# Optimization experiments

Measured on AMD Instinct MI355X. Metric: run time of the kernel, lower is better.

Reference implementation:

```python
import jax, jax.numpy as jnp
import numpy as np

B, N_PER, C, KG, KTOP, KNN = 8, 2048, 256, 16, 512, 32
N = B * N_PER
E = N * KG
EPS = 1e-5


def setup_inputs() -> dict:
    key = jax.random.key(0)
    ks = jax.random.split(key, 32)
    s = 0.05
    x = jax.random.normal(ks[0], (N, C), jnp.float32)
    x_origin = jax.random.normal(ks[1], (N, C), jnp.float32)
    xyz = jax.random.uniform(ks[2], (N, 3), jnp.float32)
    # graph: every node is a dst with KG incoming edges from random nodes of the SAME sample
    edge_dst = jnp.repeat(jnp.arange(N, dtype=jnp.int32), KG)
    src_local = jax.random.randint(ks[3], (E,), 0, N_PER, dtype=jnp.int32)
    edge_src = src_local + (edge_dst // N_PER) * N_PER
    # EdgeConv params (theta on x_j - x_i, phi on x_i)
    theta_w = jax.random.normal(ks[4], (C, C), jnp.float32) * s
    theta_b = jax.random.normal(ks[5], (C,), jnp.float32) * s
    phi_w = jax.random.normal(ks[6], (C, C), jnp.float32) * s
    phi_b = jax.random.normal(ks[7], (C,), jnp.float32) * s
    # region_score_mlp: Conv1d(C,64,1)-ReLU-BN(64)-Conv1d(64,32,1)-ReLU-BN(32)-Conv1d(32,1,1)
    w1 = jax.random.normal(ks[8], (64, C), jnp.float32) * s
    b1 = jax.random.normal(ks[9], (64,), jnp.float32) * s
    g1 = 1.0 + 0.1 * jax.random.normal(ks[10], (64,), jnp.float32)
    be1 = 0.1 * jax.random.normal(ks[11], (64,), jnp.float32)
    m1 = 0.1 * jax.random.normal(ks[12], (64,), jnp.float32)
    v1 = jax.random.uniform(ks[13], (64,), jnp.float32, 0.5, 1.5)
    w2 = jax.random.normal(ks[14], (32, 64), jnp.float32) * s
    b2 = jax.random.normal(ks[15], (32,), jnp.float32) * s
    g2 = 1.0 + 0.1 * jax.random.normal(ks[16], (32,), jnp.float32)
    be2 = 0.1 * jax.random.normal(ks[17], (32,), jnp.float32)
    m2 = 0.1 * jax.random.normal(ks[18], (32,), jnp.float32)
    v2 = jax.random.uniform(ks[19], (32,), jnp.float32, 0.5, 1.5)
    w3 = jax.random.normal(ks[20], (1, 32), jnp.float32) * s
    b3 = jax.random.normal(ks[21], (1,), jnp.float32) * s
    return dict(x=x, x_origin=x_origin, xyz=xyz, edge_src=edge_src, edge_dst=edge_dst,
                theta_w=theta_w, theta_b=theta_b, phi_w=phi_w, phi_b=phi_b,
                w1=w1, b1=b1, g1=g1, be1=be1, m1=m1, v1=v1,
                w2=w2, b2=b2, g2=g2, be2=be2, m2=m2, v2=v2, w3=w3, b3=b3)


def _bn(t, g, b, m, v):
    return (t - m) * jax.lax.rsqrt(v + EPS) * g + b


def _forward(x, x_origin, xyz, edge_src, edge_dst,
             theta_w, theta_b, phi_w, phi_b,
             w1, b1, g1, be1, m1, v1, w2, b2, g2, be2, m2, v2, w3, b3):
    # EdgeConv: h_i = max_{j->i}( theta(x_j - x_i) + phi(x_i) ), then residual add
    msg = ((x[edge_src] - x[edge_dst]) @ theta_w.T + theta_b
           + x[edge_dst] @ phi_w.T + phi_b)                      # [E, C]
    h = jax.ops.segment_max(msg, edge_dst, num_segments=N)       # [N, C]
    x1 = h + x                                                   # residual
    # per-node MLP (Conv1d kernel-size 1 == linear), BN in eval mode
    t = _bn(jax.nn.relu(x1 @ w1.T + b1), g1, be1, m1, v1)
    t = _bn(jax.nn.relu(t @ w2.T + b2), g2, be2, m2, v2)
    score = t @ w3.T + b3                                        # [N, 1]
    score_b = score.reshape(B, N_PER)                            # vps_score
    # per-batch top-k (cls=False path: select by raw score, descending)
    topk_vals, topk_idx = jax.lax.top_k(score_b, KTOP)           # [B, KTOP]
    perm = (topk_idx + jnp.arange(B, dtype=topk_idx.dtype)[:, None] * N_PER).reshape(-1)
    x_new = x1[perm].reshape(B, KTOP, C)
    x_copy = x_origin[perm].reshape(B, KTOP, -1)
    xyz_sel = xyz[perm].reshape(B, KTOP, 3)
    # rebuild 32-NN graph per sample on selected points (batched, no per-b python calls)
    d2 = jnp.sum((xyz_sel[:, :, None, :] - xyz_sel[:, None, :, :]) ** 2, axis=-1)  # [B,K,K]
    _, knn_idx = jax.lax.top_k(-d2, KNN)                         # [B, KTOP, 32]
    return knn_idx, x_new, x_copy, score_b, topk_vals


def reference(x, x_origin, xyz, edge_src, edge_dst,
              theta_w, theta_b, phi_w, phi_b,
              w1, b1, g1, be1, m1, v1, w2, b2, g2, be2, m2, v2, w3, b3):
    return _forward(x, x_origin, xyz, edge_src, edge_dst,
                    theta_w, theta_b, phi_w, phi_b,
                    w1, b1, g1, be1, m1, v1, w2, b2, g2, be2, m2, v2, w3, b3)
```

## Files before the change

### kernel.cpp

```cpp
#include <hip/hip_runtime.h>
#include <math.h>

constexpr int B     = 8;
constexpr int N_PER = 2048;
constexpr int C     = 256;
constexpr int KG    = 16;
constexpr int KTOP  = 512;
constexpr int KNN   = 32;
constexpr int N     = B * N_PER;
constexpr float EPS = 1e-5f;

typedef __attribute__((ext_vector_type(8))) short  short8;
typedef __attribute__((ext_vector_type(4))) float  f32x4;

__device__ inline void split3(float f, unsigned short& h, unsigned short& m,
                              unsigned short& l)
{
    const unsigned u  = __float_as_uint(f);
    const unsigned r1 = (u + 0x7FFFu + ((u >> 16) & 1u)) & 0xFFFF0000u;
    h = (unsigned short)(r1 >> 16);
    const float f2 = f - __uint_as_float(r1);
    const unsigned u2 = __float_as_uint(f2);
    const unsigned r2 = (u2 + 0x7FFFu + ((u2 >> 16) & 1u)) & 0xFFFF0000u;
    m = (unsigned short)(r2 >> 16);
    const float f3 = f2 - __uint_as_float(r2);
    const unsigned u3 = __float_as_uint(f3);
    l = (unsigned short)((u3 + 0x7FFFu + ((u3 >> 16) & 1u)) >> 16);
}

__device__ inline void cvt_store24(unsigned short* dh, unsigned short* dm,
                                   unsigned short* dl, float4 a, float4 b)
{
    short8 h, m, l;
    unsigned short hh, mm, ll;
    float v[8] = {a.x, a.y, a.z, a.w, b.x, b.y, b.z, b.w};
#pragma unroll
    for (int j = 0; j < 8; ++j) {
        split3(v[j], hh, mm, ll);
        h[j] = (short)hh;
        m[j] = (short)mm;
        l[j] = (short)ll;
    }
    *(short8*)dh = h;
    *(short8*)dm = m;
    *(short8*)dl = l;
}

__device__ inline void split8v(const float* __restrict__ s,
                               unsigned short* __restrict__ dh,
                               unsigned short* __restrict__ dm,
                               unsigned short* __restrict__ dl)
{
    float4 a = *(const float4*)s;
    float4 b = *(const float4*)(s + 4);
    float v[8] = {a.x, a.y, a.z, a.w, b.x, b.y, b.z, b.w};
    short8 h8, m8, l8;
    unsigned short hh, mm, ll;
#pragma unroll
    for (int j = 0; j < 8; ++j) {
        split3(v[j], hh, mm, ll);
        h8[j] = (short)hh;
        m8[j] = (short)mm;
        l8[j] = (short)ll;
    }
    *(short8*)dh = h8;
    *(short8*)dm = m8;
    *(short8*)dl = l8;
}

constexpr int GW = C * C / 8;

__global__ __launch_bounds__(256) void k0w_split(
    const float* __restrict__ thw, const float* __restrict__ phw,
    unsigned short* __restrict__ th, unsigned short* __restrict__ tm,
    unsigned short* __restrict__ tl,
    unsigned short* __restrict__ ph, unsigned short* __restrict__ pm,
    unsigned short* __restrict__ pl)
{
    const int g = blockIdx.x * 256 + threadIdx.x;
    if (g < GW) {
        const int o = g * 8;
        split8v(thw + o, th + o, tm + o, tl + o);
    } else if (g < 2 * GW) {
        const int o = (g - GW) * 8;
        split8v(phw + o, ph + o, pm + o, pl + o);
    }
}

__global__ __launch_bounds__(256) void k1_wp(
    const float* __restrict__ x,
    const unsigned short* __restrict__ th, const unsigned short* __restrict__ tm,
    const unsigned short* __restrict__ tl,
    const unsigned short* __restrict__ ph, const unsigned short* __restrict__ pm,
    const unsigned short* __restrict__ pl,
    const float* __restrict__ thb, const float* __restrict__ phb,
    float* __restrict__ T, float* __restrict__ R)
{
    constexpr int BM = 128, BN = 64, ST = 40;
    __shared__ unsigned short sA[3][BM * ST];
    __shared__ unsigned short sT[3][BN * ST];
    __shared__ unsigned short sP[3][BN * ST];

    const int tid  = threadIdx.x;
    const int row0 = blockIdx.x * BM;
    const int n0   = blockIdx.y * BN;
    const int lane = tid & 63;
    const int wv   = tid >> 6;
    const int wr   = (wv >> 1) * 64;
    const int wc   = (wv & 1) * 32;
    const int fr   = lane & 15;
    const int fk   = (lane >> 4) * 8;
    const int ar0  = tid >> 2;
    const int ac   = (tid & 3) * 8;

    f32x4 acTh[4][2], acTl[4][2], acQh[4][2], acQl[4][2];
    const f32x4 zz = {0.f, 0.f, 0.f, 0.f};
#pragma unroll
    for (int m = 0; m < 4; ++m)
#pragma unroll
        for (int n = 0; n < 2; ++n) {
            acTh[m][n] = zz; acTl[m][n] = zz;
            acQh[m][n] = zz; acQl[m][n] = zz;
        }

    const float* xA0 = x + (size_t)(row0 + ar0)      * C + ac;
    const float* xA1 = x + (size_t)(row0 + 64 + ar0) * C + ac;
    const size_t offW = (size_t)(n0 + ar0) * C + ac;

    float4 a0a = *(const float4*)(xA0 + 0), a0b = *(const float4*)(xA0 + 4);
    float4 a1a = *(const float4*)(xA1 + 0), a1b = *(const float4*)(xA1 + 4);
    short8 rTh = *(const short8*)(th + offW);
    short8 rTm = *(const short8*)(tm + offW);
    short8 rTl = *(const short8*)(tl + offW);
    short8 rPh = *(const short8*)(ph + offW);
    short8 rPm = *(const short8*)(pm + offW);
    short8 rPl = *(const short8*)(pl + offW);

    const int sOffA0 = ar0 * ST + ac;
    const int sOffA1 = (64 + ar0) * ST + ac;
    const int aBase  = (wr + fr) * ST + fk;
    const int bBase  = (wc + fr) * ST + fk;

    for (int step = 0; step < 8; ++step) {
        __syncthreads();
        cvt_store24(sA[0] + sOffA0, sA[1] + sOffA0, sA[2] + sOffA0, a0a, a0b);
        cvt_store24(sA[0] + sOffA1, sA[1] + sOffA1, sA[2] + sOffA1, a1a, a1b);
        *(short8*)(sT[0] + sOffA0) = rTh;
        *(short8*)(sT[1] + sOffA0) = rTm;
        *(short8*)(sT[2] + sOffA0) = rTl;
        *(short8*)(sP[0] + sOffA0) = rPh;
        *(short8*)(sP[1] + sOffA0) = rPm;
        *(short8*)(sP[2] + sOffA0) = rPl;
        __syncthreads();

        if (step < 7) {
            const int kn = (step + 1) * 32;
            a0a = *(const float4*)(xA0 + kn); a0b = *(const float4*)(xA0 + kn + 4);
            a1a = *(const float4*)(xA1 + kn); a1b = *(const float4*)(xA1 + kn + 4);
            rTh = *(const short8*)(th + offW + kn);
            rTm = *(const short8*)(tm + offW + kn);
            rTl = *(const short8*)(tl + offW + kn);
            rPh = *(const short8*)(ph + offW + kn);
            rPm = *(const short8*)(pm + offW + kn);
            rPl = *(const short8*)(pl + offW + kn);
        }

        short8 a1f[4], a2f[4], a3f[4];
#pragma unroll
        for (int m = 0; m < 4; ++m) {
            const int r = aBase + m * 16 * ST;
            a1f[m] = *(const short8*)(sA[0] + r);
            a2f[m] = *(const short8*)(sA[1] + r);
            a3f[m] = *(const short8*)(sA[2] + r);
        }
        {
            short8 t0[2], p0[2];
#pragma unroll
            for (int n = 0; n < 2; ++n) {
                const int r = bBase + n * 16 * ST;
                t0[n] = *(const short8*)(sT[0] + r);
                p0[n] = *(const short8*)(sP[0] + r);
            }
#pragma unroll
            for (int m = 0; m < 4; ++m)
#pragma unroll
                for (int n = 0; n < 2; ++n) {
                    acTh[m][n] = __builtin_amdgcn_mfma_f32_16x16x32_bf16(a1f[m], t0[n], acTh[m][n], 0, 0, 0);
                    acQh[m][n] = __builtin_amdgcn_mfma_f32_16x16x32_bf16(a1f[m], p0[n], acQh[m][n], 0, 0, 0);
                    acTl[m][n] = __builtin_amdgcn_mfma_f32_16x16x32_bf16(a2f[m], t0[n], acTl[m][n], 0, 0, 0);
                    acQl[m][n] = __builtin_amdgcn_mfma_f32_16x16x32_bf16(a2f[m], p0[n], acQl[m][n], 0, 0, 0);
                    acTl[m][n] = __builtin_amdgcn_mfma_f32_16x16x32_bf16(a3f[m], t0[n], acTl[m][n], 0, 0, 0);
                    acQl[m][n] = __builtin_amdgcn_mfma_f32_16x16x32_bf16(a3f[m], p0[n], acQl[m][n], 0, 0, 0);
                }
        }
        {
            short8 t1[2], p1[2];
#pragma unroll
            for (int n = 0; n < 2; ++n) {
                const int r = bBase + n * 16 * ST;
                t1[n] = *(const short8*)(sT[1] + r);
                p1[n] = *(const short8*)(sP[1] + r);
            }
#pragma unroll
            for (int m = 0; m < 4; ++m)
#pragma unroll
                for (int n = 0; n < 2; ++n) {
                    acTl[m][n] = __builtin_amdgcn_mfma_f32_16x16x32_bf16(a1f[m], t1[n], acTl[m][n], 0, 0, 0);
                    acQl[m][n] = __builtin_amdgcn_mfma_f32_16x16x32_bf16(a1f[m], p1[n], acQl[m][n], 0, 0, 0);
                    acTl[m][n] = __builtin_amdgcn_mfma_f32_16x16x32_bf16(a2f[m], t1[n], acTl[m][n], 0, 0, 0);
                    acQl[m][n] = __builtin_amdgcn_mfma_f32_16x16x32_bf16(a2f[m], p1[n], acQl[m][n], 0, 0, 0);
                }
        }
        {
            short8 t2[2], p2[2];
#pragma unroll
            for (int n = 0; n < 2; ++n) {
                const int r = bBase + n * 16 * ST;
                t2[n] = *(const short8*)(sT[2] + r);
                p2[n] = *(const short8*)(sP[2] + r);
            }
#pragma unroll
            for (int m = 0; m < 4; ++m)
#pragma unroll
                for (int n = 0; n < 2; ++n) {
                    acTl[m][n] = __builtin_amdgcn_mfma_f32_16x16x32_bf16(a1f[m], t2[n], acTl[m][n], 0, 0, 0);
                    acQl[m][n] = __builtin_amdgcn_mfma_f32_16x16x32_bf16(a1f[m], p2[n], acQl[m][n], 0, 0, 0);
                }
        }
    }

    const int cr = (lane >> 4) * 4;
#pragma unroll
    for (int m = 0; m < 4; ++m) {
#pragma unroll
        for (int n = 0; n < 2; ++n) {
            const int col  = n0 + wc + n * 16 + fr;
            const float bias = thb[col] + phb[col];
#pragma unroll
            for (int j = 0; j < 4; ++j) {
                const int row = row0 + wr + m * 16 + cr + j;
                const size_t off = (size_t)row * C + col;
                const float tval = acTh[m][n][j] + acTl[m][n][j];
                const float qval = acQh[m][n][j] + acQl[m][n][j];
                T[off] = tval;
                R[off] = x[off] + qval + bias - tval;
            }
        }
    }
}

__global__ __launch_bounds__(256) void k1_fb(
    const float* __restrict__ x, const float* __restrict__ thw,
    const float* __restrict__ phw, const float* __restrict__ thb,
    const float* __restrict__ phb, float* __restrict__ T, float* __restrict__ R)
{
    constexpr int BM = 128, BN = 64, ST = 40;
    __shared__ unsigned short sA[3][BM * ST];
    __shared__ unsigned short sT[3][BN * ST];
    __shared__ unsigned short sP[3][BN * ST];

    const int tid  = threadIdx.x;
    const int row0 = blockIdx.x * BM;
    const int n0   = blockIdx.y * BN;
    const int lane = tid & 63;
    const int wv   = tid >> 6;
    const int wr   = (wv >> 1) * 64;
    const int wc   = (wv & 1) * 32;
    const int fr   = lane & 15;
    const int fk   = (lane >> 4) * 8;
    const int ar0 = tid >> 2;
    const int ac  = (tid & 3) * 8;

    f32x4 acTh[4][2], acTl[4][2], acQh[4][2], acQl[4][2];
    const f32x4 zz = {0.f, 0.f, 0.f, 0.f};
#pragma unroll
    for (int m = 0; m < 4; ++m)
#pragma unroll
        for (int n = 0; n < 2; ++n) {
            acTh[m][n] = zz; acTl[m][n] = zz;
            acQh[m][n] = zz; acQl[m][n] = zz;
        }

    const float* xA0 = x   + (size_t)(row0 + ar0)      * C + ac;
    const float* xA1 = x   + (size_t)(row0 + 64 + ar0) * C + ac;
    const float* wT  = thw + (size_t)(n0 + ar0)        * C + ac;
    const float* wP  = phw + (size_t)(n0 + ar0)        * C + ac;

    float4 a0a = *(const float4*)(xA0 + 0), a0b = *(const float4*)(xA0 + 4);
    float4 a1a = *(const float4*)(xA1 + 0), a1b = *(const float4*)(xA1 + 4);
    float4 ta  = *(const float4*)(wT  + 0), tb_ = *(const float4*)(wT  + 4);
    float4 pa  = *(const float4*)(wP  + 0), pb_ = *(const float4*)(wP  + 4);

    const int sOffA0 = ar0 * ST + ac;
    const int sOffA1 = (64 + ar0) * ST + ac;
    const int aBase  = (wr + fr) * ST + fk;
    const int bBase  = (wc + fr) * ST + fk;

    for (int step = 0; step < 8; ++step) {
        __syncthreads();
        cvt_store24(sA[0] + sOffA0, sA[1] + sOffA0, sA[2] + sOffA0, a0a, a0b);
        cvt_store24(sA[0] + sOffA1, sA[1] + sOffA1, sA[2] + sOffA1, a1a, a1b);
        cvt_store24(sT[0] + sOffA0, sT[1] + sOffA0, sT[2] + sOffA0, ta,  tb_);
        cvt_store24(sP[0] + sOffA0, sP[1] + sOffA0, sP[2] + sOffA0, pa,  pb_);
        __syncthreads();

        if (step < 7) {
            const int kn = (step + 1) * 32;
            a0a = *(const float4*)(xA0 + kn); a0b = *(const float4*)(xA0 + kn + 4);
            a1a = *(const float4*)(xA1 + kn); a1b = *(const float4*)(xA1 + kn + 4);
            ta  = *(const float4*)(wT  + kn); tb_ = *(const float4*)(wT  + kn + 4);
            pa  = *(const float4*)(wP  + kn); pb_ = *(const float4*)(wP  + kn + 4);
        }

        short8 a1f[4], a2f[4], a3f[4];
#pragma unroll
        for (int m = 0; m < 4; ++m) {
            const int r = aBase + m * 16 * ST;
            a1f[m] = *(const short8*)(sA[0] + r);
            a2f[m] = *(const short8*)(sA[1] + r);
            a3f[m] = *(const short8*)(sA[2] + r);
        }
        {
            short8 t0[2], p0[2];
#pragma unroll
            for (int n = 0; n < 2; ++n) {
                const int r = bBase + n * 16 * ST;
                t0[n] = *(const short8*)(sT[0] + r);
                p0[n] = *(const short8*)(sP[0] + r);
            }
#pragma unroll
            for (int m = 0; m < 4; ++m)
#pragma unroll
                for (int n = 0; n < 2; ++n) {
                    acTh[m][n] = __builtin_amdgcn_mfma_f32_16x16x32_bf16(a1f[m], t0[n], acTh[m][n], 0, 0, 0);
                    acQh[m][n] = __builtin_amdgcn_mfma_f32_16x16x32_bf16(a1f[m], p0[n], acQh[m][n], 0, 0, 0);
                    acTl[m][n] = __builtin_amdgcn_mfma_f32_16x16x32_bf16(a2f[m], t0[n], acTl[m][n], 0, 0, 0);
                    acQl[m][n] = __builtin_amdgcn_mfma_f32_16x16x32_bf16(a2f[m], p0[n], acQl[m][n], 0, 0, 0);
                    acTl[m][n] = __builtin_amdgcn_mfma_f32_16x16x32_bf16(a3f[m], t0[n], acTl[m][n], 0, 0, 0);
                    acQl[m][n] = __builtin_amdgcn_mfma_f32_16x16x32_bf16(a3f[m], p0[n], acQl[m][n], 0, 0, 0);
                }
        }
        {
            short8 t1[2], p1[2];
#pragma unroll
            for (int n = 0; n < 2; ++n) {
                const int r = bBase + n * 16 * ST;
                t1[n] = *(const short8*)(sT[1] + r);
                p1[n] = *(const short8*)(sP[1] + r);
            }
#pragma unroll
            for (int m = 0; m < 4; ++m)
#pragma unroll
                for (int n = 0; n < 2; ++n) {
                    acTl[m][n] = __builtin_amdgcn_mfma_f32_16x16x32_bf16(a1f[m], t1[n], acTl[m][n], 0, 0, 0);
                    acQl[m][n] = __builtin_amdgcn_mfma_f32_16x16x32_bf16(a1f[m], p1[n], acQl[m][n], 0, 0, 0);
                    acTl[m][n] = __builtin_amdgcn_mfma_f32_16x16x32_bf16(a2f[m], t1[n], acTl[m][n], 0, 0, 0);
                    acQl[m][n] = __builtin_amdgcn_mfma_f32_16x16x32_bf16(a2f[m], p1[n], acQl[m][n], 0, 0, 0);
                }
        }
        {
            short8 t2[2], p2[2];
#pragma unroll
            for (int n = 0; n < 2; ++n) {
                const int r = bBase + n * 16 * ST;
                t2[n] = *(const short8*)(sT[2] + r);
                p2[n] = *(const short8*)(sP[2] + r);
            }
#pragma unroll
            for (int m = 0; m < 4; ++m)
#pragma unroll
                for (int n = 0; n < 2; ++n) {
                    acTl[m][n] = __builtin_amdgcn_mfma_f32_16x16x32_bf16(a1f[m], t2[n], acTl[m][n], 0, 0, 0);
                    acQl[m][n] = __builtin_amdgcn_mfma_f32_16x16x32_bf16(a1f[m], p2[n], acQl[m][n], 0, 0, 0);
                }
        }
    }

    const int cr = (lane >> 4) * 4;
#pragma unroll
    for (int m = 0; m < 4; ++m) {
#pragma unroll
        for (int n = 0; n < 2; ++n) {
            const int col  = n0 + wc + n * 16 + fr;
            const float bias = thb[col] + phb[col];
#pragma unroll
            for (int j = 0; j < 4; ++j) {
                const int row = row0 + wr + m * 16 + cr + j;
                const size_t off = (size_t)row * C + col;
                const float tval = acTh[m][n][j] + acTl[m][n][j];
                const float qval = acQh[m][n][j] + acQl[m][n][j];
                T[off] = tval;
                R[off] = x[off] + qval + bias - tval;
            }
        }
    }
}

__global__ __launch_bounds__(256) void k2ab_fused(
    const int* __restrict__ esrc, const float* __restrict__ T,
    float* __restrict__ x1,
    const float* __restrict__ w1, const float* __restrict__ b1,
    const float* __restrict__ g1, const float* __restrict__ be1,
    const float* __restrict__ m1, const float* __restrict__ v1,
    const float* __restrict__ w2, const float* __restrict__ b2,
    const float* __restrict__ g2, const float* __restrict__ be2,
    const float* __restrict__ m2, const float* __restrict__ v2,
    const float* __restrict__ w3, const float* __restrict__ b3,
    float* __restrict__ score_ws, float* __restrict__ out_score)
{
    constexpr int BK = 16, ST = 68;
    __shared__ float Xs[BK * ST];
    __shared__ float Ws[BK * ST];
    __shared__ float t1s[64 * 65];
    __shared__ float w2s[32 * 65];
    __shared__ float w3s[32];
    __shared__ float zs[64 * 33];
    __shared__ int eidx[64][KG];

    const int tid  = threadIdx.x;
    const int bb   = blockIdx.x & 7;
    const int row0 = bb * N_PER + (blockIdx.x >> 3) * 64;

#pragma unroll
    for (int q = 0; q < 4; ++q) {
        const int i = tid + q * 256;
        eidx[i >> 4][i & 15] = esrc[(row0 + (i >> 4)) * KG + (i & 15)];
    }
    __syncthreads();

    {
        const int w = tid >> 6, c4 = (tid & 63) * 4;
        for (int it = 0; it < 16; ++it) {
            const int nl = w * 16 + it;
            const int g  = row0 + nl;
            float4 acc = make_float4(-INFINITY, -INFINITY, -INFINITY, -INFINITY);
#pragma unroll
            for (int k = 0; k < KG; ++k) {
                const float4 v = *(const float4*)&T[(size_t)eidx[nl][k] * C + c4];
                acc.x = fmaxf(acc.x, v.x);  acc.y = fmaxf(acc.y, v.y);
                acc.z = fmaxf(acc.z, v.z);  acc.w = fmaxf(acc.w, v.w);
            }
            const size_t off = (size_t)g * C + c4;
            float4 r = *(const float4*)&x1[off];
            r.x += acc.x;  r.y += acc.y;  r.z += acc.z;  r.w += acc.w;
            *(float4*)&x1[off] = r;
        }
    }
    __syncthreads();

    const int tx = tid & 15, ty = tid >> 4;
    const int lm = tid >> 2, lq = (tid & 3) << 2;

    float acc[4][4] = {{0.f}};
    for (int k0 = 0; k0 < C; k0 += BK) {
        float4 fx = *(const float4*)(x1 + (size_t)(row0 + lm) * C + k0 + lq);
        float4 fw = *(const float4*)(w1 + (size_t)lm * C + k0 + lq);
        __syncthreads();
        Xs[(lq + 0) * ST + lm] = fx.x;  Xs[(lq + 1) * ST + lm] = fx.y;
        Xs[(lq + 2) * ST + lm] = fx.z;  Xs[(lq + 3) * ST + lm] = fx.w;
        Ws[(lq + 0) * ST + lm] = fw.x;  Ws[(lq + 1) * ST + lm] = fw.y;
        Ws[(lq + 2) * ST + lm] = fw.z;  Ws[(lq + 3) * ST + lm] = fw.w;
        __syncthreads();
#pragma unroll
        for (int k = 0; k < BK; ++k) {
            float4 a4 = *(const float4*)&Xs[k * ST + (ty << 2)];
            float4 w4 = *(const float4*)&Ws[k * ST + (tx << 2)];
            float av[4] = {a4.x, a4.y, a4.z, a4.w};
            float wv[4] = {w4.x, w4.y, w4.z, w4.w};
#pragma unroll
            for (int i2 = 0; i2 < 4; ++i2)
#pragma unroll
                for (int j2 = 0; j2 < 4; ++j2) acc[i2][j2] += av[i2] * wv[j2];
        }
    }
    __syncthreads();
#pragma unroll
    for (int i2 = 0; i2 < 4; ++i2) {
        const int mrow = (ty << 2) + i2;
#pragma unroll
        for (int j2 = 0; j2 < 4; ++j2) {
            const int o = (tx << 2) + j2;
            float y = acc[i2][j2] + b1[o];
            y = fmaxf(y, 0.f);
            y = (y - m1[o]) * (1.0f / sqrtf(v1[o] + EPS)) * g1[o] + be1[o];
            t1s[mrow * 65 + o] = y;
        }
    }
    for (int idx = tid; idx < 2048; idx += 256)
        w2s[(idx >> 6) * 65 + (idx & 63)] = w2[idx];
    if (tid < 32) w3s[tid] = w3[tid];
    __syncthreads();

    const int o = tid & 31;
    const float inv2 = (1.0f / sqrtf(v2[o] + EPS)) * g2[o];
#pragma unroll
    for (int p = 0; p < 8; ++p) {
        const int nl = p * 8 + (tid >> 5);
        float z = 0.f;
#pragma unroll
        for (int j = 0; j < 64; ++j) z += t1s[nl * 65 + j] * w2s[o * 65 + j];
        z += b2[o];
        z = fmaxf(z, 0.f);
        z = (z - m2[o]) * inv2 + be2[o];
        zs[nl * 33 + o] = z;
    }
    __syncthreads();

    if (tid < 64) {
        float sacc = 0.f;
#pragma unroll
        for (int j = 0; j < 32; ++j) sacc += zs[tid * 33 + j] * w3s[j];
        sacc += b3[0];
        const int node = row0 + tid;
        score_ws[node]  = sacc;
        out_score[node] = sacc;
    }
}

__global__ __launch_bounds__(256) void k3_rank(
    const float* __restrict__ score, const float* __restrict__ xyz,
    float* __restrict__ out_topk, int* __restrict__ perm,
    float* __restrict__ xsel)
{
    __shared__ unsigned long long keys[N_PER];
    const int b   = blockIdx.x >> 3;
    const int seg = blockIdx.x & 7;
    const int t   = threadIdx.x;
    for (int i = t; i < N_PER; i += 256) {
        const float v = score[b * N_PER + i];
        unsigned u = __float_as_uint(v);
        const unsigned ua = (u & 0x80000000u) ? ~u : (u | 0x80000000u);
        const unsigned ud = ~ua;
        keys[i] = ((unsigned long long)ud << 32) | (unsigned)i;
    }
    __syncthreads();
    const int i = seg * 256 + t;
    const unsigned long long k = keys[i];
    int r = 0;
#pragma unroll 8
    for (int j = 0; j < N_PER; ++j) r += (keys[j] < k) ? 1 : 0;
    if (r < KTOP) {
        const int g = b * N_PER + i;
        const int o = b * KTOP + r;
        out_topk[o] = score[g];
        perm[o] = g;
        xsel[o * 3 + 0] = xyz[g * 3 + 0];
        xsel[o * 3 + 1] = xyz[g * 3 + 1];
        xsel[o * 3 + 2] = xyz[g * 3 + 2];
    }
}

__device__ inline unsigned long long shfl_xor_u64(unsigned long long v, int m)
{
    unsigned lo = (unsigned)v, hi = (unsigned)(v >> 32);
    lo = __shfl_xor(lo, m, 64);
    hi = __shfl_xor(hi, m, 64);
    return ((unsigned long long)hi << 32) | lo;
}

__global__ __launch_bounds__(256) void k5_rank(
    const int* __restrict__ perm, const float* __restrict__ xsel,
    const float* __restrict__ x1, const float* __restrict__ xorig,
    float* __restrict__ out_xnew, float* __restrict__ out_xcopy,
    float* __restrict__ out_knn)
{
    constexpr int G = 4;
    __shared__ float px[KTOP], py[KTOP], pz[KTOP];
    const int t  = threadIdx.x;
    const int q0 = blockIdx.x * G;
    const int b  = q0 >> 9;
    const int i0 = q0 & 511;

    for (int idx = t; idx < KTOP; idx += 256) {
        const size_t base = ((size_t)b * KTOP + idx) * 3;
        px[idx] = xsel[base + 0];
        py[idx] = xsel[base + 1];
        pz[idx] = xsel[base + 2];
    }
#pragma unroll
    for (int p = 0; p < G; ++p) {
        const int row = q0 + p;
        const int g = perm[row];
        out_xnew [(size_t)row * C + t] = x1   [(size_t)g * C + t];
        out_xcopy[(size_t)row * C + t] = xorig[(size_t)g * C + t];
    }
    __syncthreads();

    const int w    = t >> 6;
    const int lane = t & 63;
    const int q    = i0 + w;
    const float qx = px[q], qy = py[q], qz = pz[q];

    unsigned long long arr[8];
#pragma unroll
    for (int e = 0; e < 8; ++e) {
        const int j = lane + 64 * e;
        const float dx = __fsub_rn(qx, px[j]);
        const float dy = __fsub_rn(qy, py[j]);
        const float dz = __fsub_rn(qz, pz[j]);
        const float d2 = __fadd_rn(__fadd_rn(__fmul_rn(dx, dx), __fmul_rn(dy, dy)),
                                   __fmul_rn(dz, dz));
        arr[e] = ((unsigned long long)__float_as_uint(d2) << 32) | (unsigned)j;
    }
#pragma unroll
    for (int pass = 0; pass < 7; ++pass)
#pragma unroll
        for (int i = 0; i < 7; ++i) {
            if (i < 7 - pass) {
                const unsigned long long a = arr[i], c = arr[i + 1];
                arr[i]     = (a < c) ? a : c;
                arr[i + 1] = (a < c) ? c : a;
            }
        }
    float* dst = out_knn + (size_t)(q0 + w) * KNN;
    for (int r = 0; r < KNN; ++r) {
        unsigned long long m = arr[0];
#pragma unroll
        for (int off = 32; off; off >>= 1) {
            const unsigned long long o = shfl_xor_u64(m, off);
            m = (o < m) ? o : m;
        }
        if (arr[0] == m) {
            dst[r] = (float)(unsigned)(m & 0xffffffffu);
#pragma unroll
            for (int i = 0; i < 7; ++i) arr[i] = arr[i + 1];
            arr[7] = ~0ull;
        }
    }
}

extern "C" void kernel_launch(void* const* d_in, const int* in_sizes, int n_in,
                              void* d_out, int out_size, void* d_ws, size_t ws_size,
                              hipStream_t stream)
{
    const float* x     = (const float*)d_in[0];
    const float* xorig = (const float*)d_in[1];
    const float* xyz   = (const float*)d_in[2];
    const int*   esrc  = (const int*)d_in[3];
    const float* thw = (const float*)d_in[5];
    const float* thb = (const float*)d_in[6];
    const float* phw = (const float*)d_in[7];
    const float* phb = (const float*)d_in[8];
    const float* w1  = (const float*)d_in[9];
    const float* b1  = (const float*)d_in[10];
    const float* g1  = (const float*)d_in[11];
    const float* be1 = (const float*)d_in[12];
    const float* m1  = (const float*)d_in[13];
    const float* v1  = (const float*)d_in[14];
    const float* w2  = (const float*)d_in[15];
    const float* b2  = (const float*)d_in[16];
    const float* g2  = (const float*)d_in[17];
    const float* be2 = (const float*)d_in[18];
    const float* m2  = (const float*)d_in[19];
    const float* v2  = (const float*)d_in[20];
    const float* w3  = (const float*)d_in[21];
    const float* b3  = (const float*)d_in[22];

    float* ws   = (float*)d_ws;
    float* T    = ws;
    float* x1   = ws + (size_t)N * C;
    float* sc   = ws + 2 * (size_t)N * C;
    int*   perm = (int*)(sc + N);
    float* xsel = (float*)(perm + B * KTOP);

    unsigned short* th = (unsigned short*)(xsel + (size_t)B * KTOP * 3);
    unsigned short* tm = th + (size_t)C * C;
    unsigned short* tl = tm + (size_t)C * C;
    unsigned short* ph = tl + (size_t)C * C;
    unsigned short* pm = ph + (size_t)C * C;
    unsigned short* pl = pm + (size_t)C * C;
    const size_t ws_need = (size_t)((char*)(pl + (size_t)C * C) - (char*)ws);
    const bool planes_ok = (ws_size >= ws_need);

    float* out     = (float*)d_out;
    float* o_knn   = out;
    float* o_xnew  = o_knn + (size_t)B * KTOP * KNN;
    float* o_xcopy = o_xnew + (size_t)B * KTOP * C;
    float* o_score = o_xcopy + (size_t)B * KTOP * C;
    float* o_topk  = o_score + (size_t)B * N_PER;

    if (planes_ok) {
        k0w_split<<<(2 * GW + 255) / 256, 256, 0, stream>>>(
            thw, phw, th, tm, tl, ph, pm, pl);
        k1_wp<<<dim3(N / 128, C / 64), 256, 0, stream>>>(
            x, th, tm, tl, ph, pm, pl, thb, phb, T, x1);
    } else {
        k1_fb<<<dim3(N / 128, C / 64), 256, 0, stream>>>(x, thw, phw, thb, phb, T, x1);
    }
    k2ab_fused<<<N / 64, 256, 0, stream>>>(esrc, T, x1,
                                           w1, b1, g1, be1, m1, v1,
                                           w2, b2, g2, be2, m2, v2, w3, b3,
                                           sc, o_score);
    k3_rank<<<8 * B, 256, 0, stream>>>(sc, xyz, o_topk, perm, xsel);
    k5_rank<<<B * KTOP / 4, 256, 0, stream>>>(perm, xsel, x1, xorig,
                                              o_xnew, o_xcopy, o_knn);
}
```

Before: 254.3 us.

## Shrink fused aggregation+MLP block to 16 nodes for more blocks

The fused edge-max aggregation and score-MLP kernel now handles 16 nodes per block instead of 64, launching four times as many blocks. The intent is more parallelism and latency hiding for the gather-heavy max aggregation, plus lower shared memory per block. The cost is that the 64x256 w1 tile and the w2 weights are reloaded by four times as many blocks, and the first GEMM drops from 4x4 to 1x4 register tiles per thread, so arithmetic intensity falls.

```diff
diff --git a/kernel.cpp b/kernel.cpp
--- a/kernel.cpp
+++ b/kernel.cpp
@@ -408,30 +408,26 @@
     const float* __restrict__ w3, const float* __restrict__ b3,
     float* __restrict__ score_ws, float* __restrict__ out_score)
 {
-    constexpr int BK = 16, ST = 68;
-    __shared__ float Xs[BK * ST];
-    __shared__ float Ws[BK * ST];
-    __shared__ float t1s[64 * 65];
+    constexpr int BK = 16, STW = 68, STX = 17, NB = 16;
+    __shared__ float Xs[BK * STX];
+    __shared__ float Ws[BK * STW];
+    __shared__ float t1s[NB * 65];
     __shared__ float w2s[32 * 65];
     __shared__ float w3s[32];
-    __shared__ float zs[64 * 33];
-    __shared__ int eidx[64][KG];
+    __shared__ float zs[NB * 33];
+    __shared__ int eidx[NB][KG];
 
     const int tid  = threadIdx.x;
     const int bb   = blockIdx.x & 7;
-    const int row0 = bb * N_PER + (blockIdx.x >> 3) * 64;
-
-#pragma unroll
-    for (int q = 0; q < 4; ++q) {
-        const int i = tid + q * 256;
-        eidx[i >> 4][i & 15] = esrc[(row0 + (i >> 4)) * KG + (i & 15)];
-    }
+    const int row0 = bb * N_PER + (blockIdx.x >> 3) * NB;
+
+    eidx[tid >> 4][tid & 15] = esrc[(row0 + (tid >> 4)) * KG + (tid & 15)];
     __syncthreads();
 
     {
         const int w = tid >> 6, c4 = (tid & 63) * 4;
-        for (int it = 0; it < 16; ++it) {
-            const int nl = w * 16 + it;
+        for (int it = 0; it < 4; ++it) {
+            const int nl = w * 4 + it;
             const int g  = row0 + nl;
             float4 acc = make_float4(-INFINITY, -INFINITY, -INFINITY, -INFINITY);
 #pragma unroll
@@ -449,42 +445,38 @@
     __syncthreads();
 
     const int tx = tid & 15, ty = tid >> 4;
-    const int lm = tid >> 2, lq = (tid & 3) << 2;
-
-    float acc[4][4] = {{0.f}};
+    float acc[4] = {0.f, 0.f, 0.f, 0.f};
     for (int k0 = 0; k0 < C; k0 += BK) {
-        float4 fx = *(const float4*)(x1 + (size_t)(row0 + lm) * C + k0 + lq);
+        float4 fx;
+        if (tid < 64)
+            fx = *(const float4*)(x1 + (size_t)(row0 + (tid >> 2)) * C + k0 + ((tid & 3) << 2));
+        const int lm = tid >> 2, lq = (tid & 3) << 2;
         float4 fw = *(const float4*)(w1 + (size_t)lm * C + k0 + lq);
         __syncthreads();
-        Xs[(lq + 0) * ST + lm] = fx.x;  Xs[(lq + 1) * ST + lm] = fx.y;
-        Xs[(lq + 2) * ST + lm] = fx.z;  Xs[(lq + 3) * ST + lm] = fx.w;
-        Ws[(lq + 0) * ST + lm] = fw.x;  Ws[(lq + 1) * ST + lm] = fw.y;
-        Ws[(lq + 2) * ST + lm] = fw.z;  Ws[(lq + 3) * ST + lm] = fw.w;
+        if (tid < 64) {
+            const int xr = tid >> 2, xq = (tid & 3) << 2;
+            Xs[(xq + 0) * STX + xr] = fx.x;  Xs[(xq + 1) * STX + xr] = fx.y;
+            Xs[(xq + 2) * STX + xr] = fx.z;  Xs[(xq + 3) * STX + xr] = fx.w;
+        }
+        Ws[(lq + 0) * STW + lm] = fw.x;  Ws[(lq + 1) * STW + lm] = fw.y;
+        Ws[(lq + 2) * STW + lm] = fw.z;  Ws[(lq + 3) * STW + lm] = fw.w;
         __syncthreads();
 #pragma unroll
         for (int k = 0; k < BK; ++k) {
-            float4 a4 = *(const float4*)&Xs[k * ST + (ty << 2)];
-            float4 w4 = *(const float4*)&Ws[k * ST + (tx << 2)];
-            float av[4] = {a4.x, a4.y, a4.z, a4.w};
-            float wv[4] = {w4.x, w4.y, w4.z, w4.w};
-#pragma unroll
-            for (int i2 = 0; i2 < 4; ++i2)
-#pragma unroll
-                for (int j2 = 0; j2 < 4; ++j2) acc[i2][j2] += av[i2] * wv[j2];
+            const float av = Xs[k * STX + ty];
+            const float4 w4 = *(const float4*)&Ws[k * STW + (tx << 2)];
+            acc[0] += av * w4.x;  acc[1] += av * w4.y;
+            acc[2] += av * w4.z;  acc[3] += av * w4.w;
         }
     }
     __syncthreads();
 #pragma unroll
-    for (int i2 = 0; i2 < 4; ++i2) {
-        const int mrow = (ty << 2) + i2;
-#pragma unroll
-        for (int j2 = 0; j2 < 4; ++j2) {
-            const int o = (tx << 2) + j2;
-            float y = acc[i2][j2] + b1[o];
-            y = fmaxf(y, 0.f);
-            y = (y - m1[o]) * (1.0f / sqrtf(v1[o] + EPS)) * g1[o] + be1[o];
-            t1s[mrow * 65 + o] = y;
-        }
+    for (int j2 = 0; j2 < 4; ++j2) {
+        const int o = (tx << 2) + j2;
+        float y = acc[j2] + b1[o];
+        y = fmaxf(y, 0.f);
+        y = (y - m1[o]) * (1.0f / sqrtf(v1[o] + EPS)) * g1[o] + be1[o];
+        t1s[ty * 65 + o] = y;
     }
     for (int idx = tid; idx < 2048; idx += 256)
         w2s[(idx >> 6) * 65 + (idx & 63)] = w2[idx];
@@ -494,7 +486,7 @@
     const int o = tid & 31;
     const float inv2 = (1.0f / sqrtf(v2[o] + EPS)) * g2[o];
 #pragma unroll
-    for (int p = 0; p < 8; ++p) {
+    for (int p = 0; p < 2; ++p) {
         const int nl = p * 8 + (tid >> 5);
         float z = 0.f;
 #pragma unroll
@@ -506,7 +498,7 @@
     }
     __syncthreads();
 
-    if (tid < 64) {
+    if (tid < NB) {
         float sacc = 0.f;
 #pragma unroll
         for (int j = 0; j < 32; ++j) sacc += zs[tid * 33 + j] * w3s[j];
@@ -687,7 +679,7 @@
     } else {
         k1_fb<<<dim3(N / 128, C / 64), 256, 0, stream>>>(x, thw, phw, thb, phb, T, x1);
     }
-    k2ab_fused<<<N / 64, 256, 0, stream>>>(esrc, T, x1,
+    k2ab_fused<<<N / 16, 256, 0, stream>>>(esrc, T, x1,
                                            w1, b1, g1, be1, m1, v1,
                                            w2, b2, g2, be2, m2, v2, w3, b3,
                                            sc, o_score);
```

Result: faster. 243.0 us (median of 2 runs) (-4.5%).
